# Kernel optimization log

Measured on AMD Instinct MI355X. Metric: run time of the kernel, lower is better.

## Reference

```python
import jax, jax.numpy as jnp
import numpy as np
from jax import lax

PAD = (2, 1)        # pad=(2,1) from init, applied to both H and W
UPSAMPLE_F = 2      # kernel scaled by upsample_f**2


def make_kernel(k1d, upsample_f):
    k = jnp.asarray(k1d, dtype=jnp.float32)
    k = k[None, :] * k[:, None]          # 1D -> separable 2D outer product
    k = k / jnp.sum(k)                   # normalize to sum 1
    if upsample_f > 1:
        k = k * (upsample_f ** 2)
    return k                             # [4, 4]


def setup_inputs() -> dict:
    key = jax.random.key(0)
    x = jax.random.normal(key, (16, 512, 64, 64), dtype=jnp.float32)
    kernel = make_kernel([1, 3, 3, 1], UPSAMPLE_F)
    return {"x": x, "kernel": kernel}


def reference(x, kernel):
    # upfirdn2d(x, kernel, up=1, down=1, pad=(2,1)):
    # pad H and W by (2,1), then TRUE convolution (kernel flipped) applied
    # depthwise (same FIR kernel on every channel).
    n, c, h, w = x.shape
    kh, kw = kernel.shape
    wflip = jnp.flip(kernel, (0, 1))                     # true conv = flip + correlate
    wdw = jnp.broadcast_to(wflip[None, None], (c, 1, kh, kw))  # [C,1,kh,kw] depthwise
    out = lax.conv_general_dilated(
        x, wdw,
        window_strides=(1, 1),
        padding=(PAD, PAD),
        feature_group_count=c,
        dimension_numbers=("NCHW", "OIHW", "NCHW"),
    )
    return out  # [N, C, H, W] (same spatial size: 64+2+1-4+1 = 64)
```

## Files before the change

### kernel.cpp

```cpp
#include <hip/hip_runtime.h>


#define PH 64
#define PW 64
#define LDW 68

__global__ __launch_bounds__(256) void blur_sep_kernel(
    const float* __restrict__ x, float* __restrict__ out) {
    __shared__ float s_in[PH * LDW];
    __shared__ float s_tmp[PH * LDW];

    const int plane = blockIdx.x;
    const int t = threadIdx.x;

    const float* __restrict__ src = x + (size_t)plane * (PH * PW);
    float* __restrict__ dst = out + (size_t)plane * (PH * PW);

    #pragma unroll
    for (int k = 0; k < 4; ++k) {
        const int f = t + k * 256;
        const float4 v = reinterpret_cast<const float4*>(src)[f];
        const int y = f >> 4;
        const int x0 = (f & 15) << 2;
        float4* p = reinterpret_cast<float4*>(&s_in[y * LDW + x0]);
        *p = v;
    }
    __syncthreads();

    {
        const int r = t >> 2;
        const int xseg = (t & 3) << 4;
        const float* __restrict__ row = &s_in[r * LDW];
        float* __restrict__ trow = &s_tmp[r * LDW];
        #pragma unroll
        for (int i = 0; i < 16; ++i) {
            const int xx = xseg + i;
            const float a = (xx >= 2)      ? row[xx - 2] : 0.0f;
            const float b = (xx >= 1)      ? row[xx - 1] : 0.0f;
            const float c = row[xx];
            const float d = (xx + 1 < PW)  ? row[xx + 1] : 0.0f;
            trow[xx] = 0.25f * (a + d) + 0.75f * (b + c);
        }
    }
    __syncthreads();

    #pragma unroll
    for (int k = 0; k < 4; ++k) {
        const int f = t + k * 256;
        const int y = f >> 4;
        const int x0 = (f & 15) << 2;
        float acc0 = 0.f, acc1 = 0.f, acc2 = 0.f, acc3 = 0.f;
        #pragma unroll
        for (int i = 0; i < 4; ++i) {
            const int yy = y + i - 2;
            if (yy >= 0 && yy < PH) {
                const float wgt = (i == 0 || i == 3) ? 0.25f : 0.75f;
                const float* __restrict__ trow = &s_tmp[yy * LDW + x0];
                acc0 += wgt * trow[0];
                acc1 += wgt * trow[1];
                acc2 += wgt * trow[2];
                acc3 += wgt * trow[3];
            }
        }
        float4 v;
        v.x = acc0; v.y = acc1; v.z = acc2; v.w = acc3;
        reinterpret_cast<float4*>(dst)[f] = v;
    }
}

extern "C" void kernel_launch(void* const* d_in, const int* in_sizes, int n_in,
                              void* d_out, int out_size, void* d_ws, size_t ws_size,
                              hipStream_t stream) {
    const float* x = (const float*)d_in[0];
    float* out = (float*)d_out;
    const int nplanes = in_sizes[0] / (PH * PW);
    blur_sep_kernel<<<nplanes, 256, 0, stream>>>(x, out);
}
```

Measured before the change: 45.85 us.

## Replace shared-memory separable blur with register sliding window and lane shuffles

Measured after the change: 49.80 us. 8.6% more time.

```diff
diff --git a/kernel.cpp b/kernel.cpp
--- a/kernel.cpp
+++ b/kernel.cpp
@@ -1,70 +1,53 @@
 #include <hip/hip_runtime.h>
 
 
+#define PW 64
 #define PH 64
-#define PW 64
-#define LDW 68
+#define CHUNK 16
 
-__global__ __launch_bounds__(256) void blur_sep_kernel(
+__global__ __launch_bounds__(256) void blur_shfl_kernel(
     const float* __restrict__ x, float* __restrict__ out) {
-    __shared__ float s_in[PH * LDW];
-    __shared__ float s_tmp[PH * LDW];
+    const int t = threadIdx.x;
+    const int lane16 = t & 15;
+    const int grp = t >> 4;
+    const int y0 = (grp >> 2) * CHUNK;
+    const int plane = blockIdx.x * 4 + (grp & 3);
 
-    const int plane = blockIdx.x;
-    const int t = threadIdx.x;
+    const float* __restrict__ src = x + (size_t)plane * (PH * PW) + lane16 * 4;
+    float* __restrict__ dst = out + (size_t)plane * (PH * PW) + lane16 * 4;
 
-    const float* __restrict__ src = x + (size_t)plane * (PH * PW);
-    float* __restrict__ dst = out + (size_t)plane * (PH * PW);
+    float4 hA = make_float4(0.f, 0.f, 0.f, 0.f);
+    float4 hB = hA, hC = hA;
 
     #pragma unroll
-    for (int k = 0; k < 4; ++k) {
-        const int f = t + k * 256;
-        const float4 v = reinterpret_cast<const float4*>(src)[f];
-        const int y = f >> 4;
-        const int x0 = (f & 15) << 2;
-        float4* p = reinterpret_cast<float4*>(&s_in[y * LDW + x0]);
-        *p = v;
-    }
-    __syncthreads();
+    for (int i = 0; i < CHUNK + 3; ++i) {
+        const int y = y0 - 2 + i;
+        float4 v = make_float4(0.f, 0.f, 0.f, 0.f);
+        if (y >= 0 && y < PH) {
+            v = *reinterpret_cast<const float4*>(src + y * PW);
+        }
 
-    {
-        const int r = t >> 2;
-        const int xseg = (t & 3) << 4;
-        const float* __restrict__ row = &s_in[r * LDW];
-        float* __restrict__ trow = &s_tmp[r * LDW];
-        #pragma unroll
-        for (int i = 0; i < 16; ++i) {
-            const int xx = xseg + i;
-            const float a = (xx >= 2)      ? row[xx - 2] : 0.0f;
-            const float b = (xx >= 1)      ? row[xx - 1] : 0.0f;
-            const float c = row[xx];
-            const float d = (xx + 1 < PW)  ? row[xx + 1] : 0.0f;
-            trow[xx] = 0.25f * (a + d) + 0.75f * (b + c);
+        float pz = __shfl_up(v.z, 1, 16);
+        float pw = __shfl_up(v.w, 1, 16);
+        float nx = __shfl_down(v.x, 1, 16);
+        if (lane16 == 0)  { pz = 0.f; pw = 0.f; }
+        if (lane16 == 15) { nx = 0.f; }
+        float4 hD;
+        hD.x = 0.75f * (pw  + v.x) + 0.25f * (pz  + v.y);
+        hD.y = 0.75f * (v.x + v.y) + 0.25f * (pw  + v.z);
+        hD.z = 0.75f * (v.y + v.z) + 0.25f * (v.x + v.w);
+        hD.w = 0.75f * (v.z + v.w) + 0.25f * (v.y + nx);
+
+        if (i >= 3) {
+            const int yo = y - 1;
+            float4 o;
+            o.x = 0.25f * (hA.x + hD.x) + 0.75f * (hB.x + hC.x);
+            o.y = 0.25f * (hA.y + hD.y) + 0.75f * (hB.y + hC.y);
+            o.z = 0.25f * (hA.z + hD.z) + 0.75f * (hB.z + hC.z);
+            o.w = 0.25f * (hA.w + hD.w) + 0.75f * (hB.w + hC.w);
+            *reinterpret_cast<float4*>(dst + yo * PW) = o;
         }
-    }
-    __syncthreads();
-
-    #pragma unroll
-    for (int k = 0; k < 4; ++k) {
-        const int f = t + k * 256;
-        const int y = f >> 4;
-        const int x0 = (f & 15) << 2;
-        float acc0 = 0.f, acc1 = 0.f, acc2 = 0.f, acc3 = 0.f;
-        #pragma unroll
-        for (int i = 0; i < 4; ++i) {
-            const int yy = y + i - 2;
-            if (yy >= 0 && yy < PH) {
-                const float wgt = (i == 0 || i == 3) ? 0.25f : 0.75f;
-                const float* __restrict__ trow = &s_tmp[yy * LDW + x0];
-                acc0 += wgt * trow[0];
-                acc1 += wgt * trow[1];
-                acc2 += wgt * trow[2];
-                acc3 += wgt * trow[3];
-            }
-        }
-        float4 v;
-        v.x = acc0; v.y = acc1; v.z = acc2; v.w = acc3;
-        reinterpret_cast<float4*>(dst)[f] = v;
+        hA = hB; hB = hC; hC = hD;
     }
 }
 
@@ -74,5 +57,5 @@
     const float* x = (const float*)d_in[0];
     float* out = (float*)d_out;
     const int nplanes = in_sizes[0] / (PH * PW);
-    blur_sep_kernel<<<nplanes, 256, 0, stream>>>(x, out);
+    blur_shfl_kernel<<<nplanes / 4, 256, 0, stream>>>(x, out);
 }
```
